# Kernel tuning notes

Measured on AMD Instinct MI355X. Metric: run time of the kernel, lower is better.

The kernel has to match this reference:

```python
import jax, jax.numpy as jnp
import numpy as np
from jax import lax

DN = ('NCHW', 'OIHW', 'NCHW')

def _conv(x, w, b, stride, pad):
    y = lax.conv_general_dilated(x, w, (stride, stride), [(pad, pad), (pad, pad)], dimension_numbers=DN)
    return y + b[None, :, None, None]

def _resblock(x, w1, b1, w2, b2, wd, bd, stride):
    # standard pre-activation-free ResNet block: conv3x3(stride)-ReLU-conv3x3 + 1x1(stride) skip, final ReLU
    identity = _conv(x, wd, bd, stride, 0)
    h = jax.nn.relu(_conv(x, w1, b1, stride, 1))
    h = _conv(h, w2, b2, 1, 1)
    return jax.nn.relu(h + identity)

def _deconv(x, w, b, stride, out_pad):
    # PyTorch ConvTranspose2d(k=3, padding=1, output_padding=out_pad) as dilated conv
    # w has PyTorch layout (in_ch, out_ch, kH, kW) -> flip spatially, swap to OIHW
    wt = jnp.flip(w, (2, 3)).transpose(1, 0, 2, 3)
    y = lax.conv_general_dilated(x, wt, (1, 1), [(1, 1 + out_pad), (1, 1 + out_pad)], lhs_dilation=(stride, stride), dimension_numbers=DN)
    return y + b[None, :, None, None]

def _quantize(enc, codebook):
    # enc: (B, C, H, W); codebook: (N, C). Squared-Euclidean distances, argmin, lookup.
    e = enc.transpose(0, 2, 3, 1)  # (B, H, W, C)
    d = (jnp.sum(e * e, axis=-1, keepdims=True)
         - 2.0 * jnp.einsum('bhwc,nc->bhwn', e, codebook)
         + jnp.sum(codebook * codebook, axis=-1))  # (B, H, W, N)
    idx = jnp.argmin(d, axis=-1)
    q = codebook[idx]  # (B, H, W, C)
    return q.transpose(0, 3, 1, 2)

def setup_inputs() -> dict:
    key = jax.random.key(0)
    ks = jax.random.split(key, 28)
    def W(k, shape):
        return jax.random.normal(k, shape, jnp.float32) * 0.05
    inp = {"x": jax.random.normal(ks[0], (32, 3, 256, 256), jnp.float32)}
    enc_chans = [(3, 64), (64, 128), (128, 64)]
    i = 1
    for l, (cin, cout) in enumerate(enc_chans):
        inp[f"enc{l}_w1"] = W(ks[i], (cout, cin, 3, 3))
        inp[f"enc{l}_b1"] = W(ks[i + 1], (cout,))
        inp[f"enc{l}_w2"] = W(ks[i + 2], (cout, cout, 3, 3))
        inp[f"enc{l}_b2"] = W(ks[i + 3], (cout,))
        inp[f"enc{l}_wd"] = W(ks[i + 4], (cout, cin, 1, 1))
        inp[f"enc{l}_bd"] = W(ks[i + 5], (cout,))
        i += 6
    # decoder ConvTranspose2d weights in PyTorch layout (in_ch, out_ch, 3, 3)
    dec_chans = [(64, 128), (128, 64), (64, 3)]
    for l, (cin, cout) in enumerate(dec_chans):
        inp[f"dec{l}_w"] = W(ks[i], (cin, cout, 3, 3))
        inp[f"dec{l}_b"] = W(ks[i + 1], (cout,))
        i += 2
    inp["codebook"] = W(ks[i], (512, 64))
    return inp

def reference(x, enc0_w1, enc0_b1, enc0_w2, enc0_b2, enc0_wd, enc0_bd,
              enc1_w1, enc1_b1, enc1_w2, enc1_b2, enc1_wd, enc1_bd,
              enc2_w1, enc2_b1, enc2_w2, enc2_b2, enc2_wd, enc2_bd,
              dec0_w, dec0_b, dec1_w, dec1_b, dec2_w, dec2_b, codebook):
    # encode: 256 -> 128 -> 64 -> 64 spatially
    h = _resblock(x, enc0_w1, enc0_b1, enc0_w2, enc0_b2, enc0_wd, enc0_bd, 2)
    h = _resblock(h, enc1_w1, enc1_b1, enc1_w2, enc1_b2, enc1_wd, enc1_bd, 2)
    h = _resblock(h, enc2_w1, enc2_b1, enc2_w2, enc2_b2, enc2_wd, enc2_bd, 1)
    q = _quantize(h, codebook)
    # decode with output_size matching encoder input shapes (output_padding: 0, 1, 1)
    h = jax.nn.relu(_deconv(q, dec0_w, dec0_b, 1, 0))   # 64 -> 64
    h = jax.nn.relu(_deconv(h, dec1_w, dec1_b, 2, 1))   # 64 -> 128
    return _deconv(h, dec2_w, dec2_b, 2, 1)             # 128 -> 256
```

## Files before the change

### kernel.cpp

```cpp
#include <hip/hip_runtime.h>
#include <cstddef>


typedef float v4f __attribute__((ext_vector_type(4)));
typedef _Float16 f16x8 __attribute__((ext_vector_type(8)));
typedef _Float16 f16x4 __attribute__((ext_vector_type(4)));

__device__ __forceinline__ void fma4(v4f& a, float p, const v4f& w) {
    a.x = fmaf(p, w.x, a.x); a.y = fmaf(p, w.y, a.y);
    a.z = fmaf(p, w.z, a.z); a.w = fmaf(p, w.w, a.w);
}

__global__ void repack_k(const float* __restrict__ src, float* __restrict__ dst,
                         int cout, int coutR, int cin, int flip, int deconv)
{
    int t = blockIdx.x * 256 + threadIdx.x;
    int tot = cin * 9 * cout;
    if (t >= tot) return;
    int co = t % cout; int k = (t / cout) % 9; int ci = t / (9 * cout);
    float v = 0.f;
    if (co < coutR) {
        int ks = flip ? 8 - k : k;
        v = deconv ? src[((size_t)ci * coutR + co) * 9 + ks]
                   : src[((size_t)co * cin + ci) * 9 + ks];
    }
    dst[t] = v;
}

__global__ void repackB16_k(const float* __restrict__ src, _Float16* __restrict__ bh,
                            _Float16* __restrict__ bl, int COUT, int CIN, int deconv)
{
    int t = blockIdx.x * 256 + threadIdx.x;
    int tot = 9 * CIN * COUT;
    if (t >= tot) return;
    int NGtot = COUT >> 4, C32 = CIN >> 5;
    int j = t & 7;
    int lane = (t >> 3) & 63;
    int blk = t >> 9;
    int ng = blk % NGtot; blk /= NGtot;
    int c32 = blk % C32;
    int tap = blk / C32;
    int co = ng * 16 + (lane & 15);
    int ci = c32 * 32 + ((lane >> 4) & 3) * 8 + j;
    float v = deconv ? src[((size_t)ci * COUT + co) * 9 + (8 - tap)]
                     : src[((size_t)co * CIN + ci) * 9 + tap];
    _Float16 h = (_Float16)v;
    _Float16 l = (_Float16)(v - (float)h);
    bh[t] = h; bl[t] = l;
}

__global__ void repackW16_k(const float* __restrict__ src, _Float16* __restrict__ wh,
                            _Float16* __restrict__ wl, int COUT, int CIN)
{
    int t = blockIdx.x * 256 + threadIdx.x;
    int tot = CIN * COUT;
    if (t >= tot) return;
    int NGtot = COUT >> 4;
    int j = t & 7;
    int lane = (t >> 3) & 63;
    int blk = t >> 9;
    int ng = blk % NGtot;
    int c32 = blk / NGtot;
    int co = ng * 16 + (lane & 15);
    int ci = c32 * 32 + ((lane >> 4) & 3) * 8 + j;
    float v = src[(size_t)co * CIN + ci];
    _Float16 h = (_Float16)v;
    wh[t] = h; wl[t] = (_Float16)(v - (float)h);
}

__global__ void repackQ_k(const float* __restrict__ cb, _Float16* __restrict__ qb)
{
    int t = blockIdx.x * 256 + threadIdx.x;
    if (t >= 65536) return;
    int j = t & 7;
    int lane = (t >> 3) & 63;
    int hl = (t >> 9) & 1;
    int s = (t >> 10) & 1;
    int nt = t >> 11;
    int code = nt * 16 + (lane & 15);
    int ci = s * 32 + ((lane >> 4) & 3) * 8 + j;
    float v = cb[(size_t)code * 64 + ci];
    _Float16 h = (_Float16)v;
    qb[t] = hl ? (_Float16)(v - (float)h) : h;
}

__global__ void cbnorm_k(const float* __restrict__ cb, float* __restrict__ cn)
{
    int i = blockIdx.x * 256 + threadIdx.x;
    if (i >= 512) return;
    float s = 0.f;
#pragma unroll
    for (int j = 0; j < 64; ++j) { float v = cb[i * 64 + j]; s = fmaf(v, v, s); }
    cn[i] = s;
}

template<int CIN, bool RELU, int ADDMODE, bool CLIN, bool CLOUT>
__launch_bounds__(256, 2)
__global__ void mconv3s1_k(const float* __restrict__ in,
                           const _Float16* __restrict__ Bh, const _Float16* __restrict__ Bl,
                           const float* __restrict__ bias, float* __restrict__ out,
                           const float* __restrict__ addend,
                           int COUT, int H, int W)
{
    constexpr int C32 = CIN / 32;
    __shared__ __align__(16) unsigned char smBuf[76416];
    _Float16* AH = (_Float16*)smBuf;
    _Float16* AL = AH + 12960;
    _Float16* BW = AL + 12960;
    float* smO = (float*)smBuf;

    const int tid = threadIdx.x;
    const int lane = tid & 63, yb = tid >> 6;
    const int n16 = lane & 15, q = lane >> 4;

    int b = blockIdx.x;
    const int chunks = COUT >> 6;
    const int coch = b % chunks; b /= chunks;
    const int tX = W >> 4; const int tx = b % tX; b /= tX;
    const int tY = H >> 4; const int ty = b % tY; const int n = b / tY;
    const int x0 = tx * 16, y0 = ty * 16;
    const int NGtot = COUT >> 4;
    const int ngbase = coch * 4, cobase = coch * 64;

    v4f acc[4][4];
#pragma unroll
    for (int ng = 0; ng < 4; ++ng) {
        float bb = bias[cobase + ng * 16 + n16];
        v4f bv = {bb, bb, bb, bb};
#pragma unroll
        for (int mg = 0; mg < 4; ++mg) acc[mg][ng] = bv;
    }

    for (int c32 = 0; c32 < C32; ++c32) {
        __syncthreads();
        if (CLIN) {
            for (int u = tid; u < 2592; u += 256) {
                int cell = u >> 3, f4 = u & 7;
                int yy = cell / 18, xx = cell - yy * 18;
                int gy = y0 - 1 + yy, gx = x0 - 1 + xx;
                float4 v = make_float4(0.f, 0.f, 0.f, 0.f);
                if (gy >= 0 && gy < H && gx >= 0 && gx < W)
                    v = *(const float4*)&in[(((size_t)n * H + gy) * W + gx) * CIN + c32 * 32 + f4 * 4];
                f16x4 h4, l4;
                h4[0] = (_Float16)v.x; l4[0] = (_Float16)(v.x - (float)h4[0]);
                h4[1] = (_Float16)v.y; l4[1] = (_Float16)(v.y - (float)h4[1]);
                h4[2] = (_Float16)v.z; l4[2] = (_Float16)(v.z - (float)h4[2]);
                h4[3] = (_Float16)v.w; l4[3] = (_Float16)(v.w - (float)h4[3]);
                int a = (yy * 18 + xx) * 40 + f4 * 4;
                *(f16x4*)&AH[a] = h4; *(f16x4*)&AL[a] = l4;
            }
        } else {
            for (int u = tid; u < 10368; u += 256) {
                int ci = u / 324, rem = u - ci * 324;
                int yy = rem / 18, xx = rem - yy * 18;
                int gy = y0 - 1 + yy, gx = x0 - 1 + xx;
                float v = 0.f;
                if (gy >= 0 && gy < H && gx >= 0 && gx < W)
                    v = in[(((size_t)n * CIN + c32 * 32 + ci) * H + gy) * W + gx];
                _Float16 h = (_Float16)v;
                _Float16 l = (_Float16)(v - (float)h);
                int a = (yy * 18 + xx) * 40 + ci;
                AH[a] = h; AL[a] = l;
            }
        }
        for (int ky = 0; ky < 3; ++ky) {
            __syncthreads();
            for (int u = tid; u < 1536; u += 256) {
                int lu = u & 63;
                int rest = u >> 6;
                int hl = rest & 1; rest >>= 1;
                int ng = rest & 3;
                int tapL = rest >> 2;
                const uint4* srcp = (const uint4*)(hl ? Bl : Bh);
                size_t sidx = (((size_t)(ky * 3 + tapL) * C32 + c32) * NGtot + ngbase + ng) * 64 + lu;
                ((uint4*)BW)[u] = srcp[sidx];
            }
            __syncthreads();
#pragma unroll
            for (int kx = 0; kx < 3; ++kx) {
                f16x8 aH[4], aL[4];
#pragma unroll
                for (int mg = 0; mg < 4; ++mg) {
                    int aoff = ((4 * yb + mg + ky) * 18 + n16 + kx) * 40 + q * 8;
                    aH[mg] = *(const f16x8*)&AH[aoff];
                    aL[mg] = *(const f16x8*)&AL[aoff];
                }
                __builtin_amdgcn_s_setprio(1);
#pragma unroll
                for (int ng = 0; ng < 4; ++ng) {
                    int boff = ((kx * 4 + ng) * 2) * 512 + lane * 8;
                    f16x8 bH = *(const f16x8*)&BW[boff];
                    f16x8 bL = *(const f16x8*)&BW[boff + 512];
#pragma unroll
                    for (int mg = 0; mg < 4; ++mg) {
                        acc[mg][ng] = __builtin_amdgcn_mfma_f32_16x16x32_f16(aH[mg], bH, acc[mg][ng], 0, 0, 0);
                        acc[mg][ng] = __builtin_amdgcn_mfma_f32_16x16x32_f16(aL[mg], bH, acc[mg][ng], 0, 0, 0);
                        acc[mg][ng] = __builtin_amdgcn_mfma_f32_16x16x32_f16(aH[mg], bL, acc[mg][ng], 0, 0, 0);
                    }
                }
                __builtin_amdgcn_s_setprio(0);
            }
        }
    }

    __syncthreads();
#pragma unroll
    for (int mg = 0; mg < 4; ++mg)
#pragma unroll
        for (int ng = 0; ng < 4; ++ng) {
            int p = (4 * yb + mg) * 16 + q * 4;
            int co = ng * 16 + n16;
#pragma unroll
            for (int r = 0; r < 4; ++r)
                smO[co * 257 + p + r] = acc[mg][ng][r];
        }
    __syncthreads();
    if (CLOUT) {
        const int p = tid;
        const int py = p >> 4, px = p & 15;
        size_t cellBase = (((size_t)n * H + (y0 + py)) * W + (x0 + px)) * COUT + cobase;
        float* cellp = out + cellBase;
        const float* acell = (ADDMODE == 2) ? addend + cellBase : nullptr;
#pragma unroll
        for (int g = 0; g < 16; ++g) {
            float4 v;
            v.x = smO[(4 * g + 0) * 257 + p];
            v.y = smO[(4 * g + 1) * 257 + p];
            v.z = smO[(4 * g + 2) * 257 + p];
            v.w = smO[(4 * g + 3) * 257 + p];
            if (ADDMODE == 2) {
                float4 a4 = *(const float4*)&acell[4 * g];
                v.x += a4.x; v.y += a4.y; v.z += a4.z; v.w += a4.w;
            }
            if (RELU) {
                v.x = fmaxf(v.x, 0.f); v.y = fmaxf(v.y, 0.f);
                v.z = fmaxf(v.z, 0.f); v.w = fmaxf(v.w, 0.f);
            }
            *(float4*)&cellp[4 * g] = v;
        }
    } else {
        const size_t plane = (size_t)H * W;
        float* ob = out + ((size_t)n * COUT + cobase) * plane;
        const float* ab = (ADDMODE == 1) ? addend + ((size_t)n * COUT + cobase) * plane : nullptr;
#pragma unroll
        for (int k = 0; k < 64; ++k) {
            int e = tid + 256 * k;
            int co = e >> 8, p = e & 255;
            int py = p >> 4, px = p & 15;
            size_t g = (size_t)co * plane + (size_t)(y0 + py) * W + x0 + px;
            float v = smO[co * 257 + p];
            if (ADDMODE == 1) v += ab[g];
            if (RELU) v = fmaxf(v, 0.f);
            ob[g] = v;
        }
    }
}

template<int CIN, int NG, bool RELU>
__launch_bounds__(256, 3)
__global__ void mconv3s2_k(const float* __restrict__ in,
                           const _Float16* __restrict__ Bh, const _Float16* __restrict__ Bl,
                           const float* __restrict__ bias, float* __restrict__ out,
                           const _Float16* __restrict__ Wh, const _Float16* __restrict__ Wl,
                           const float* __restrict__ bias1, float* __restrict__ out1,
                           int COUT, int Hin, int Win)
{
    constexpr int C32 = CIN / 32;
    constexpr int ASZ = 9 * 2 * 17 * 40;
    __shared__ __align__(16) unsigned char smBuf[2 * ASZ * 2];
    _Float16* AH = (_Float16*)smBuf;
    _Float16* AL = AH + ASZ;
    float* smO = (float*)smBuf;

    const int tid = threadIdx.x;
    const int lane = tid & 63, yb = tid >> 6;
    const int n16 = lane & 15, q = lane >> 4;

    const int Hout = Hin >> 1, Wout = Win >> 1;
    int b = blockIdx.x;
    const int chunks = COUT / (NG * 16);
    const int coch = b % chunks; b /= chunks;
    const int tX = Wout >> 4; const int tx = b % tX; b /= tX;
    const int tY = Hout >> 2; const int ty = b % tY; const int n = b / tY;
    const int x0 = tx * 16, y0 = ty * 4;
    const int gx0 = 2 * x0 - 1, gy0 = 2 * y0 - 1;
    const int NGtot = COUT >> 4;
    const int ngbase = coch * NG, cobase = coch * NG * 16;

    v4f acc[NG];
    v4f accW[NG];
#pragma unroll
    for (int ng = 0; ng < NG; ++ng) {
        float bb = bias[cobase + ng * 16 + n16];
        v4f bv = {bb, bb, bb, bb};
        acc[ng] = bv;
        float bw = bias1[cobase + ng * 16 + n16];
        v4f bwv = {bw, bw, bw, bw};
        accW[ng] = bwv;
    }

    const uint4* bhp = (const uint4*)Bh;
    const uint4* blp = (const uint4*)Bl;
    const uint4* whp = (const uint4*)Wh;
    const uint4* wlp = (const uint4*)Wl;

    for (int c32 = 0; c32 < C32; ++c32) {
        __syncthreads();
        for (int u = tid; u < 2376; u += 256) {
            int cell = u >> 3, f4 = u & 7;
            int yy = cell / 33, xx = cell - yy * 33;
            int gy = gy0 + yy, gx = gx0 + xx;
            float4 v = make_float4(0.f, 0.f, 0.f, 0.f);
            if (gy >= 0 && gy < Hin && gx >= 0 && gx < Win)
                v = *(const float4*)&in[(((size_t)n * Hin + gy) * Win + gx) * CIN + c32 * 32 + f4 * 4];
            f16x4 h4, l4;
            h4[0] = (_Float16)v.x; l4[0] = (_Float16)(v.x - (float)h4[0]);
            h4[1] = (_Float16)v.y; l4[1] = (_Float16)(v.y - (float)h4[1]);
            h4[2] = (_Float16)v.z; l4[2] = (_Float16)(v.z - (float)h4[2]);
            h4[3] = (_Float16)v.w; l4[3] = (_Float16)(v.w - (float)h4[3]);
            int a = ((yy * 2 + (xx & 1)) * 17 + (xx >> 1)) * 40 + f4 * 4;
            *(f16x4*)&AH[a] = h4; *(f16x4*)&AL[a] = l4;
        }
        __syncthreads();
#pragma unroll
        for (int ky = 0; ky < 3; ++ky) {
#pragma unroll
            for (int kx = 0; kx < 3; ++kx) {
                const int par = kx & 1, xs = kx >> 1;
                int aoff = (((2 * yb + ky) * 2 + par) * 17 + n16 + xs) * 40 + q * 8;
                f16x8 aH = *(const f16x8*)&AH[aoff];
                f16x8 aL = *(const f16x8*)&AL[aoff];
                size_t sb0 = (((size_t)(ky * 3 + kx) * C32 + c32) * NGtot + ngbase) * 64 + lane;
                __builtin_amdgcn_s_setprio(1);
#pragma unroll
                for (int ng = 0; ng < NG; ++ng) {
                    uint4 rH = bhp[sb0 + (size_t)ng * 64];
                    uint4 rL = blp[sb0 + (size_t)ng * 64];
                    f16x8 bH = *(const f16x8*)&rH;
                    f16x8 bL = *(const f16x8*)&rL;
                    acc[ng] = __builtin_amdgcn_mfma_f32_16x16x32_f16(aH, bH, acc[ng], 0, 0, 0);
                    acc[ng] = __builtin_amdgcn_mfma_f32_16x16x32_f16(aL, bH, acc[ng], 0, 0, 0);
                    acc[ng] = __builtin_amdgcn_mfma_f32_16x16x32_f16(aH, bL, acc[ng], 0, 0, 0);
                }
                __builtin_amdgcn_s_setprio(0);
                if (ky == 1 && kx == 1) {
                    size_t sw0 = ((size_t)c32 * NGtot + ngbase) * 64 + lane;
                    __builtin_amdgcn_s_setprio(1);
#pragma unroll
                    for (int ng = 0; ng < NG; ++ng) {
                        uint4 rH = whp[sw0 + (size_t)ng * 64];
                        uint4 rL = wlp[sw0 + (size_t)ng * 64];
                        f16x8 bH = *(const f16x8*)&rH;
                        f16x8 bL = *(const f16x8*)&rL;
                        accW[ng] = __builtin_amdgcn_mfma_f32_16x16x32_f16(aH, bH, accW[ng], 0, 0, 0);
                        accW[ng] = __builtin_amdgcn_mfma_f32_16x16x32_f16(aL, bH, accW[ng], 0, 0, 0);
                        accW[ng] = __builtin_amdgcn_mfma_f32_16x16x32_f16(aH, bL, accW[ng], 0, 0, 0);
                    }
                    __builtin_amdgcn_s_setprio(0);
                }
            }
        }
    }

    __syncthreads();
#pragma unroll
    for (int ng = 0; ng < NG; ++ng) {
        int co = ng * 16 + n16;
        int p = yb * 16 + q * 4;
#pragma unroll
        for (int r = 0; r < 4; ++r)
            smO[co * 65 + p + r] = acc[ng][r];
    }
    __syncthreads();
    const int p2 = tid >> 2, s2 = tid & 3;
    const int py = p2 >> 4, px = p2 & 15;
    float* cellp = out + ((((size_t)n * Hout + (y0 + py)) * Wout + (x0 + px)) * COUT + s2 * 32);
#pragma unroll
    for (int k = 0; k < 8; ++k) {
        float4 v;
        v.x = smO[(s2 * 32 + 4 * k + 0) * 65 + p2];
        v.y = smO[(s2 * 32 + 4 * k + 1) * 65 + p2];
        v.z = smO[(s2 * 32 + 4 * k + 2) * 65 + p2];
        v.w = smO[(s2 * 32 + 4 * k + 3) * 65 + p2];
        if (RELU) {
            v.x = fmaxf(v.x, 0.f); v.y = fmaxf(v.y, 0.f);
            v.z = fmaxf(v.z, 0.f); v.w = fmaxf(v.w, 0.f);
        }
        *(float4*)&cellp[4 * k] = v;
    }

    __syncthreads();
#pragma unroll
    for (int ng = 0; ng < NG; ++ng) {
        int co = ng * 16 + n16;
        int p = yb * 16 + q * 4;
#pragma unroll
        for (int r = 0; r < 4; ++r)
            smO[co * 65 + p + r] = accW[ng][r];
    }
    __syncthreads();
    float* cellp1 = out1 + ((((size_t)n * Hout + (y0 + py)) * Wout + (x0 + px)) * COUT + s2 * 32);
#pragma unroll
    for (int k = 0; k < 8; ++k) {
        float4 v;
        v.x = smO[(s2 * 32 + 4 * k + 0) * 65 + p2];
        v.y = smO[(s2 * 32 + 4 * k + 1) * 65 + p2];
        v.z = smO[(s2 * 32 + 4 * k + 2) * 65 + p2];
        v.w = smO[(s2 * 32 + 4 * k + 3) * 65 + p2];
        *(float4*)&cellp1[4 * k] = v;
    }
}

template<int CIN, bool RELU>
__launch_bounds__(256, 3)
__global__ void mdeconv2_k(const float* __restrict__ in,
                           const _Float16* __restrict__ Bh, const _Float16* __restrict__ Bl,
                           const float* __restrict__ bias, float* __restrict__ out,
                           int COUT, int Hin, int Win)
{
    constexpr int C32 = CIN / 32;
    __shared__ __align__(16) unsigned char smBuf[38976];
    _Float16* AH = (_Float16*)smBuf;
    _Float16* AL = AH + 3600;
    _Float16* BW = AL + 3600;
    float* smO = (float*)smBuf;

    const int tid = threadIdx.x;
    const int lane = tid & 63, yb = tid >> 6;
    const int n16 = lane & 15, q = lane >> 4;

    int b = blockIdx.x;
    const int chunks = COUT >> 6;
    const int coch = b % chunks; b /= chunks;
    const int tX = Win >> 4; const int tx = b % tX; b /= tX;
    const int tY = Hin >> 2; const int ty = b % tY; const int n = b / tY;
    const int x0 = tx * 16, y0 = ty * 4;
    const int NGtot = COUT >> 4;
    const int ngbase = coch * 4, cobase = coch * 64;

    v4f acc[4][4];
#pragma unroll
    for (int ng = 0; ng < 4; ++ng) {
        float bb = bias[cobase + ng * 16 + n16];
        v4f bv = {bb, bb, bb, bb};
#pragma unroll
        for (int ph = 0; ph < 4; ++ph) acc[ph][ng] = bv;
    }

    for (int c32 = 0; c32 < C32; ++c32) {
        __syncthreads();
        for (int u = tid; u < 680; u += 256) {
            int cell = u >> 3, f4 = u & 7;
            int yy = cell / 17, xx = cell - yy * 17;
            int gy = y0 + yy, gx = x0 + xx;
            float4 v = make_float4(0.f, 0.f, 0.f, 0.f);
            if (gy < Hin && gx < Win)
                v = *(const float4*)&in[(((size_t)n * Hin + gy) * Win + gx) * CIN + c32 * 32 + f4 * 4];
            f16x4 h4, l4;
            h4[0] = (_Float16)v.x; l4[0] = (_Float16)(v.x - (float)h4[0]);
            h4[1] = (_Float16)v.y; l4[1] = (_Float16)(v.y - (float)h4[1]);
            h4[2] = (_Float16)v.z; l4[2] = (_Float16)(v.z - (float)h4[2]);
            h4[3] = (_Float16)v.w; l4[3] = (_Float16)(v.w - (float)h4[3]);
            int a = (yy * 18 + xx) * 40 + f4 * 4;
            *(f16x4*)&AH[a] = h4; *(f16x4*)&AL[a] = l4;
        }
        for (int ky = 0; ky < 3; ++ky) {
            __syncthreads();
            for (int u = tid; u < 1536; u += 256) {
                int lu = u & 63;
                int rest = u >> 6;
                int hl = rest & 1; rest >>= 1;
                int ng = rest & 3;
                int tapL = rest >> 2;
                const uint4* srcp = (const uint4*)(hl ? Bl : Bh);
                size_t sidx = (((size_t)(ky * 3 + tapL) * C32 + c32) * NGtot + ngbase + ng) * 64 + lu;
                ((uint4*)BW)[u] = srcp[sidx];
            }
            __syncthreads();
            const int iy = (ky == 2) ? 1 : 0;
            const int phy = (ky == 1) ? 0 : 2;
#pragma unroll
            for (int kx = 0; kx < 3; ++kx) {
                const int ix = (kx == 2) ? 1 : 0;
                const int ph = phy + ((kx == 1) ? 0 : 1);
                int aoff = ((yb + iy) * 18 + n16 + ix) * 40 + q * 8;
                f16x8 aH = *(const f16x8*)&AH[aoff];
                f16x8 aL = *(const f16x8*)&AL[aoff];
                __builtin_amdgcn_s_setprio(1);
#pragma unroll
                for (int ng = 0; ng < 4; ++ng) {
                    int boff = ((kx * 4 + ng) * 2) * 512 + lane * 8;
                    f16x8 bH = *(const f16x8*)&BW[boff];
                    f16x8 bL = *(const f16x8*)&BW[boff + 512];
                    acc[ph][ng] = __builtin_amdgcn_mfma_f32_16x16x32_f16(aH, bH, acc[ph][ng], 0, 0, 0);
                    acc[ph][ng] = __builtin_amdgcn_mfma_f32_16x16x32_f16(aL, bH, acc[ph][ng], 0, 0, 0);
                    acc[ph][ng] = __builtin_amdgcn_mfma_f32_16x16x32_f16(aH, bL, acc[ph][ng], 0, 0, 0);
                }
                __builtin_amdgcn_s_setprio(0);
            }
        }
    }

    const int Wout = Win * 2;
    const size_t plane = (size_t)(Hin * 2) * (size_t)Wout;
    float* ob = out + ((size_t)n * COUT + cobase) * plane;
    const int oy0 = 2 * y0, ox0 = 2 * x0;
#pragma unroll
    for (int half = 0; half < 2; ++half) {
        __syncthreads();
#pragma unroll
        for (int ph = 0; ph < 4; ++ph) {
            const int dy = ph >> 1, dx = ph & 1;
#pragma unroll
            for (int g = 0; g < 2; ++g) {
                int ng = half * 2 + g;
#pragma unroll
                for (int r = 0; r < 4; ++r)
                    smO[(g * 16 + n16) * 257 + (2 * yb + dy) * 32 + 2 * (q * 4 + r) + dx] = acc[ph][ng][r];
            }
        }
        __syncthreads();
#pragma unroll
        for (int k = 0; k < 32; ++k) {
            int pos = tid;
            int oyl = pos >> 5, oxl = pos & 31;
            float v = smO[k * 257 + pos];
            if (RELU) v = fmaxf(v, 0.f);
            ob[(size_t)(half * 32 + k) * plane + (size_t)(oy0 + oyl) * Wout + ox0 + oxl] = v;
        }
    }
}

template<int CIN, int CB, bool RELU, bool FUSE>
__launch_bounds__(256, 4)
__global__ void conv3s2_k(const float* __restrict__ in, const float* __restrict__ wp,
                          const float* __restrict__ bias, float* __restrict__ out,
                          const float* __restrict__ wd, const float* __restrict__ bd,
                          float* __restrict__ out1,
                          int COUT, int Hin, int Win)
{
    constexpr int COC = 32;
    __shared__ float smIn[CB * 2178];
    __shared__ float smW[CB * 9 * COC];
    __shared__ float smWD[96];
    const int Hout = Hin >> 1, Wout = Win >> 1;
    const int tid = threadIdx.x;
    int b = blockIdx.x;
    const int chunks = COUT / COC;
    const int tX = Wout / 32, tY = Hout / 16;
    const int ch = b % chunks; b /= chunks;
    const int tx = b % tX; b /= tX;
    const int ty = b % tY; const int n = b / tY;
    const int cobase = ch * COC;
    const int r = tid >> 4, c = tid & 15;
    const int gy0 = ty * 32 - 1, gx0 = tx * 64 - 1;

    v4f acc[16];
#pragma unroll
    for (int g = 0; g < 8; ++g) {
        v4f bv = *(const v4f*)&bias[cobase + 4 * g];
        acc[g] = bv; acc[8 + g] = bv;
    }

    const size_t plane = (size_t)Hin * Win;
    const float* ip0 = in + (size_t)n * CIN * plane;
    const float* wp0 = wp + cobase;

    for (int ci0 = 0; ci0 < CIN; ci0 += CB) {
        __syncthreads();
        for (int idx = tid; idx < CB * 2178; idx += 256) {
            int ci = idx / 2178, rem = idx - ci * 2178;
            int rr = rem / 66, cc = rem - rr * 66;
            int gy = gy0 + rr, gx = gx0 + cc;
            float v = 0.f;
            if (gy >= 0 && gy < Hin && gx >= 0 && gx < Win)
                v = ip0[(size_t)(ci0 + ci) * plane + (size_t)gy * Win + gx];
            smIn[idx] = v;
        }
        for (int idx = tid; idx < CB * 9 * COC; idx += 256) {
            int q2 = idx >> 5, co = idx & 31;
            smW[idx] = wp0[((size_t)ci0 * 9 + q2) * COUT + co];
        }
        if (FUSE && tid < 96) {
            int ci = tid >> 5, co = tid & 31;
            smWD[tid] = wd[(size_t)(cobase + co) * 3 + ci];
        }
        __syncthreads();

#pragma unroll 1
        for (int ci = 0; ci < CB; ++ci) {
            float p[15];
            const float* sp = &smIn[ci * 2178 + 2 * r * 66 + 4 * c];
#pragma unroll
            for (int i = 0; i < 3; ++i)
#pragma unroll
                for (int j = 0; j < 5; ++j)
                    p[i * 5 + j] = sp[i * 66 + j];
            const float* wrow = &smW[ci * 288];
#pragma unroll
            for (int k = 0; k < 9; ++k) {
                const int ky = k / 3, kx = k % 3;
#pragma unroll
                for (int g = 0; g < 8; ++g) {
                    v4f wv = *(const v4f*)&wrow[k * 32 + 4 * g];
                    fma4(acc[g],     p[ky * 5 + kx],     wv);
                    fma4(acc[8 + g], p[ky * 5 + kx + 2], wv);
                }
            }
        }
    }

    const int oy = ty * 16 + r, ox = tx * 32 + 2 * c;
    size_t cellBase = (((size_t)n * Hout + oy) * Wout + ox) * COUT + cobase;
#pragma unroll
    for (int g = 0; g < 8; ++g) {
        v4f v0 = acc[g], v1 = acc[8 + g];
        if (RELU) {
#pragma unroll
            for (int e = 0; e < 4; ++e) { v0[e] = fmaxf(v0[e], 0.f); v1[e] = fmaxf(v1[e], 0.f); }
        }
        *(v4f*)&out[cellBase + 4 * g] = v0;
        *(v4f*)&out[cellBase + COUT + 4 * g] = v1;
    }

    if (FUSE) {
        v4f a0[8], a1[8];
#pragma unroll
        for (int g = 0; g < 8; ++g) {
            v4f bv = *(const v4f*)&bd[cobase + 4 * g];
            a0[g] = bv; a1[g] = bv;
        }
#pragma unroll
        for (int ci = 0; ci < CB; ++ci) {
            const float* sp = &smIn[ci * 2178 + 2 * r * 66 + 4 * c];
            float v0 = sp[66 + 1], v1 = sp[66 + 3];
#pragma unroll
            for (int g = 0; g < 8; ++g) {
                v4f wv = *(const v4f*)&smWD[ci * 32 + 4 * g];
                fma4(a0[g], v0, wv);
                fma4(a1[g], v1, wv);
            }
        }
        size_t cb1 = (((size_t)n * Hout + oy) * Wout + ox) * COUT + cobase;
#pragma unroll
        for (int g = 0; g < 8; ++g) {
            *(v4f*)&out1[cb1 + 4 * g] = a0[g];
            *(v4f*)&out1[cb1 + COUT + 4 * g] = a1[g];
        }
    }
}

template<int CIN, int CB, int COC, bool RELU>
__launch_bounds__(256, 3)
__global__ void deconv2_k(const float* __restrict__ in, const float* __restrict__ wp,
                          const float* __restrict__ bias, float* __restrict__ out,
                          int COUTR, int COUTP, int Hin, int Win)
{
    constexpr int RW = 33, RH = 17;
    __shared__ float smIn[CB * RH * RW];
    __shared__ float smW[CB * 9 * COC];
    const int Wout = Win * 2;
    const int tid = threadIdx.x;
    int b = blockIdx.x;
    const int chunks = COUTP / COC;
    const int qTX = Win / 32, qTY = Hin / 16;
    const int ch = b % chunks; b /= chunks;
    const int qtx = b % qTX; b /= qTX;
    const int qty = b % qTY; const int n = b / qTY;
    const int cobase = ch * COC;
    const int tqy = tid >> 4, tqx = tid & 15;
    const int qby = qty * 16, qbx = qtx * 32;

    v4f acc[8 * COC / 4];
#pragma unroll
    for (int g = 0; g < COC / 4; ++g) {
        v4f bv;
#pragma unroll
        for (int e = 0; e < 4; ++e)
            bv[e] = (cobase + 4 * g + e < COUTR) ? bias[cobase + 4 * g + e] : 0.f;
#pragma unroll
        for (int pt = 0; pt < 8; ++pt) acc[pt * (COC / 4) + g] = bv;
    }

    const size_t plane = (size_t)Hin * Win;
    const float* ip0 = in + (size_t)n * CIN * plane;
    const float* wp0 = wp + cobase;

    for (int ci0 = 0; ci0 < CIN; ci0 += CB) {
        __syncthreads();
        for (int idx = tid; idx < CB * RH * RW; idx += 256) {
            int ci = idx / (RH * RW), rem = idx - ci * (RH * RW);
            int rr = rem / RW, cc = rem - rr * RW;
            int gy = qby + rr, gx = qbx + cc;
            float v = 0.f;
            if (gy < Hin && gx < Win)
                v = ip0[(size_t)(ci0 + ci) * plane + (size_t)gy * Win + gx];
            smIn[idx] = v;
        }
        for (int idx = tid; idx < CB * 9 * COC; idx += 256) {
            int q2 = idx / COC, co = idx % COC;
            smW[idx] = wp0[((size_t)ci0 * 9 + q2) * COUTP + co];
        }
        __syncthreads();

#pragma unroll 1
        for (int ci = 0; ci < CB; ++ci) {
            float p[6];
            const float* sp = &smIn[ci * RH * RW + tqy * RW + 2 * tqx];
#pragma unroll
            for (int i = 0; i < 2; ++i)
#pragma unroll
                for (int j = 0; j < 3; ++j)
                    p[i * 3 + j] = sp[i * RW + j];
            const float* wrow = &smW[ci * 9 * COC];
#pragma unroll
            for (int k = 0; k < 9; ++k) {
                const int ky = k / 3, kx = k % 3;
                const int dy = (ky == 1) ? 0 : 1, iy = (ky == 0) ? 1 : 0;
                const int dx = (kx == 1) ? 0 : 1, ix = (kx == 0) ? 1 : 0;
#pragma unroll
                for (int g = 0; g < COC / 4; ++g) {
                    v4f wv = *(const v4f*)&wrow[k * COC + 4 * g];
                    fma4(acc[(0 + dy * 2 + dx) * (COC / 4) + g], p[iy * 3 + ix],     wv);
                    fma4(acc[(4 + dy * 2 + dx) * (COC / 4) + g], p[iy * 3 + ix + 1], wv);
                }
            }
        }
    }

    const size_t oPlane = (size_t)(Hin * 2) * Wout;
    const int oy = 2 * (qby + tqy), ox = 2 * (qbx + 2 * tqx);
#pragma unroll
    for (int g = 0; g < COC / 4; ++g)
#pragma unroll
        for (int e = 0; e < 4; ++e) {
            int cch = cobase + 4 * g + e;
            if (cch >= COUTR) break;
            float* op = out + ((size_t)n * COUTR + cch) * oPlane + (size_t)oy * Wout + ox;
#pragma unroll
            for (int a2 = 0; a2 < 2; ++a2) {
                float u0 = acc[(0 + a2 * 2 + 0) * (COC / 4) + g][e];
                float u1 = acc[(0 + a2 * 2 + 1) * (COC / 4) + g][e];
                float u2 = acc[(4 + a2 * 2 + 0) * (COC / 4) + g][e];
                float u3 = acc[(4 + a2 * 2 + 1) * (COC / 4) + g][e];
                if (RELU) { u0 = fmaxf(u0, 0.f); u1 = fmaxf(u1, 0.f);
                            u2 = fmaxf(u2, 0.f); u3 = fmaxf(u3, 0.f); }
                *(float4*)&op[(size_t)a2 * Wout] = make_float4(u0, u1, u2, u3);
            }
        }
}

template<int CIN, int S, bool RELU, bool CLIN, bool CLOUT>
__launch_bounds__(256, 4)
__global__ void conv1x1_k(const float* __restrict__ in, const float* __restrict__ w,
                          const float* __restrict__ bias, float* __restrict__ out,
                          int COUT, int Hin, int Win, int Hout, int Wout)
{
    constexpr int COC = 32;
    __shared__ float smW[CIN * COC];
    const int tid = threadIdx.x;
    int b = blockIdx.x;
    const int chunks = COUT / COC;
    const int spB = (Hout * Wout) / 256;
    const int ch = b % chunks; b /= chunks;
    const int sb = b % spB; const int n = b / spB;
    const int cobase = ch * COC;

    for (int idx = tid; idx < CIN * COC; idx += 256) {
        int ci = idx / COC, co = idx - ci * COC;
        smW[idx] = w[(size_t)(cobase + co) * CIN + ci];
    }
    __syncthreads();

    const int pos = sb * 256 + tid;
    const int oy = pos / Wout, ox = pos - oy * Wout;

    v4f acc[8];
#pragma unroll
    for (int g = 0; g < 8; ++g) acc[g] = *(const v4f*)&bias[cobase + 4 * g];

    if (CLIN) {
        const float* ip = in + (((size_t)n * Hin + oy * S) * Win + ox * S) * CIN;
#pragma unroll 1
        for (int c4 = 0; c4 < CIN / 4; ++c4) {
            v4f v = *(const v4f*)&ip[c4 * 4];
#pragma unroll
            for (int e = 0; e < 4; ++e)
#pragma unroll
                for (int g = 0; g < 8; ++g)
                    fma4(acc[g], v[e], *(const v4f*)&smW[(c4 * 4 + e) * COC + 4 * g]);
        }
    } else {
        const size_t inPlane = (size_t)Hin * Win;
        const float* ip = in + (size_t)n * CIN * inPlane + (size_t)(oy * S) * Win + (size_t)(ox * S);
#pragma unroll 1
        for (int ci = 0; ci < CIN; ++ci) {
            float v = ip[(size_t)ci * inPlane];
#pragma unroll
            for (int g = 0; g < 8; ++g)
                fma4(acc[g], v, *(const v4f*)&smW[ci * COC + 4 * g]);
        }
    }
    const size_t outPlane = (size_t)Hout * Wout;
    if (CLOUT) {
        size_t cb2 = ((size_t)n * outPlane + pos) * COUT + cobase;
#pragma unroll
        for (int g = 0; g < 8; ++g) {
            v4f v = acc[g];
            if (RELU) {
#pragma unroll
                for (int e = 0; e < 4; ++e) v[e] = fmaxf(v[e], 0.f);
            }
            *(v4f*)&out[cb2 + 4 * g] = v;
        }
    } else {
        float* op = out + ((size_t)n * COUT + cobase) * outPlane + pos;
#pragma unroll
        for (int g = 0; g < 8; ++g)
#pragma unroll
            for (int e = 0; e < 4; ++e) {
                float v = acc[g][e];
                if (RELU) v = fmaxf(v, 0.f);
                op[(size_t)(4 * g + e) * outPlane] = v;
            }
    }
}

__launch_bounds__(256, 4)
__global__ void mquant_k(const float* __restrict__ h, const _Float16* __restrict__ QB,
                         const float* __restrict__ cn, const float* __restrict__ cb,
                         float* __restrict__ q)
{
    __shared__ __align__(16) _Float16 AF[2][8192];
    __shared__ float cns[512];
    __shared__ int bidxs[128];

    const int tid = threadIdx.x;
    const int lane = tid & 63;
    const int wv = tid >> 6;
    const int n16 = lane & 15, qq = lane >> 4;

    const int n = blockIdx.x >> 5;
    const int rem0 = (blockIdx.x & 31) << 7;

    for (int u = tid; u < 1024; u += 256) {
        int posL = u >> 3, grp = u & 7;
        const float* gp = h + ((size_t)n * 4096 + rem0 + posL) * 64 + grp * 8;
        float4 v0 = *(const float4*)gp;
        float4 v1 = *(const float4*)(gp + 4);
        f16x8 hh, ll;
        hh[0] = (_Float16)v0.x; ll[0] = (_Float16)(v0.x - (float)hh[0]);
        hh[1] = (_Float16)v0.y; ll[1] = (_Float16)(v0.y - (float)hh[1]);
        hh[2] = (_Float16)v0.z; ll[2] = (_Float16)(v0.z - (float)hh[2]);
        hh[3] = (_Float16)v0.w; ll[3] = (_Float16)(v0.w - (float)hh[3]);
        hh[4] = (_Float16)v1.x; ll[4] = (_Float16)(v1.x - (float)hh[4]);
        hh[5] = (_Float16)v1.y; ll[5] = (_Float16)(v1.y - (float)hh[5]);
        hh[6] = (_Float16)v1.z; ll[6] = (_Float16)(v1.z - (float)hh[6]);
        hh[7] = (_Float16)v1.w; ll[7] = (_Float16)(v1.w - (float)hh[7]);
        int mt = posL >> 4, s = grp >> 2, qv = grp & 3;
        int a = ((mt * 2 + s) * 64 + (posL & 15) + qv * 16) * 8;
        *(f16x8*)&AF[0][a] = hh;
        *(f16x8*)&AF[1][a] = ll;
    }
    for (int u = tid; u < 512; u += 256) cns[u] = cn[u];
    __syncthreads();

    f16x8 aH[2][2], aL[2][2];
#pragma unroll
    for (int m = 0; m < 2; ++m)
#pragma unroll
        for (int s = 0; s < 2; ++s) {
            int a = (((wv * 2 + m) * 2 + s) * 64 + lane) * 8;
            aH[m][s] = *(const f16x8*)&AF[0][a];
            aL[m][s] = *(const f16x8*)&AF[1][a];
        }

    float best[2][4]; int bi[2][4];
#pragma unroll
    for (int m = 0; m < 2; ++m)
#pragma unroll
        for (int r = 0; r < 4; ++r) { best[m][r] = 3.4e38f; bi[m][r] = 0; }

    const uint4* qbp = (const uint4*)QB;
#pragma unroll 1
    for (int nt = 0; nt < 32; ++nt) {
        uint4 rH0 = qbp[((nt * 2 + 0) * 2 + 0) * 64 + lane];
        uint4 rL0 = qbp[((nt * 2 + 0) * 2 + 1) * 64 + lane];
        uint4 rH1 = qbp[((nt * 2 + 1) * 2 + 0) * 64 + lane];
        uint4 rL1 = qbp[((nt * 2 + 1) * 2 + 1) * 64 + lane];
        f16x8 bH0 = *(const f16x8*)&rH0;
        f16x8 bL0 = *(const f16x8*)&rL0;
        f16x8 bH1 = *(const f16x8*)&rH1;
        f16x8 bL1 = *(const f16x8*)&rL1;
        float cnv = cns[nt * 16 + n16];
        const int code = nt * 16 + n16;
        __builtin_amdgcn_s_setprio(1);
#pragma unroll
        for (int m = 0; m < 2; ++m) {
            v4f acc = {0.f, 0.f, 0.f, 0.f};
            acc = __builtin_amdgcn_mfma_f32_16x16x32_f16(aH[m][0], bH0, acc, 0, 0, 0);
            acc = __builtin_amdgcn_mfma_f32_16x16x32_f16(aL[m][0], bH0, acc, 0, 0, 0);
            acc = __builtin_amdgcn_mfma_f32_16x16x32_f16(aH[m][0], bL0, acc, 0, 0, 0);
            acc = __builtin_amdgcn_mfma_f32_16x16x32_f16(aH[m][1], bH1, acc, 0, 0, 0);
            acc = __builtin_amdgcn_mfma_f32_16x16x32_f16(aL[m][1], bH1, acc, 0, 0, 0);
            acc = __builtin_amdgcn_mfma_f32_16x16x32_f16(aH[m][1], bL1, acc, 0, 0, 0);
#pragma unroll
            for (int r = 0; r < 4; ++r) {
                float d = fmaf(-2.f, acc[r], cnv);
                if (d < best[m][r]) { best[m][r] = d; bi[m][r] = code; }
            }
        }
        __builtin_amdgcn_s_setprio(0);
    }

#pragma unroll
    for (int m = 0; m < 2; ++m)
#pragma unroll
        for (int r = 0; r < 4; ++r) {
#pragma unroll
            for (int msk = 1; msk < 16; msk <<= 1) {
                float ob = __shfl_xor(best[m][r], msk);
                int oi = __shfl_xor(bi[m][r], msk);
                if (ob < best[m][r] || (ob == best[m][r] && oi < bi[m][r])) {
                    best[m][r] = ob; bi[m][r] = oi;
                }
            }
            if (n16 == 0) bidxs[wv * 32 + m * 16 + qq * 4 + r] = bi[m][r];
        }
    __syncthreads();

    const int p = tid & 127, jh = tid >> 7;
    const int code = bidxs[p];
    const float4* crow4 = (const float4*)(cb + (size_t)code * 64);
    float4* qp4 = (float4*)(q + ((size_t)n * 4096 + rem0 + p) * 64);
#pragma unroll
    for (int k = 0; k < 8; ++k)
        qp4[jh * 8 + k] = crow4[jh * 8 + k];
}

extern "C" void kernel_launch(void* const* d_in, const int* in_sizes, int n_in,
                              void* d_out, int out_size, void* d_ws, size_t ws_size,
                              hipStream_t stream)
{
    const float* x    = (const float*)d_in[0];
    const float* e0w1 = (const float*)d_in[1];  const float* e0b1 = (const float*)d_in[2];
    const float* e0w2 = (const float*)d_in[3];  const float* e0b2 = (const float*)d_in[4];
    const float* e0wd = (const float*)d_in[5];  const float* e0bd = (const float*)d_in[6];
    const float* e1w1 = (const float*)d_in[7];  const float* e1b1 = (const float*)d_in[8];
    const float* e1w2 = (const float*)d_in[9];  const float* e1b2 = (const float*)d_in[10];
    const float* e1wd = (const float*)d_in[11]; const float* e1bd = (const float*)d_in[12];
    const float* e2w1 = (const float*)d_in[13]; const float* e2b1 = (const float*)d_in[14];
    const float* e2w2 = (const float*)d_in[15]; const float* e2b2 = (const float*)d_in[16];
    const float* e2wd = (const float*)d_in[17]; const float* e2bd = (const float*)d_in[18];
    const float* d0w  = (const float*)d_in[19]; const float* d0b  = (const float*)d_in[20];
    const float* d1w  = (const float*)d_in[21]; const float* d1b  = (const float*)d_in[22];
    const float* d2w  = (const float*)d_in[23]; const float* d2b  = (const float*)d_in[24];
    const float* cb   = (const float*)d_in[25];
    float* out = (float*)d_out;
    float* ws  = (float*)d_ws;

    float* P_e0w1 = out + 0;
    _Float16* Bh_d1   = (_Float16*)(out + 1728);
    _Float16* Bl_d1   = (_Float16*)(out + 38592);
    _Float16* Bh_e0c2 = (_Float16*)(out + 77760);
    _Float16* Bl_e0c2 = (_Float16*)(out + 96192);
    _Float16* Bh_e1c2 = (_Float16*)(out + 114624);
    _Float16* Bl_e1c2 = (_Float16*)(out + 188352);
    _Float16* Bh_e2c1 = (_Float16*)(out + 262080);
    _Float16* Bl_e2c1 = (_Float16*)(out + 298944);
    _Float16* Bh_e2c2 = (_Float16*)(out + 335808);
    _Float16* Bl_e2c2 = (_Float16*)(out + 354240);
    _Float16* Bh_d0   = (_Float16*)(out + 372672);
    _Float16* Bl_d0   = (_Float16*)(out + 409536);
    _Float16* Bh_e1c1 = (_Float16*)(out + 446400);
    _Float16* Bl_e1c1 = (_Float16*)(out + 483264);
    _Float16* QB = (_Float16*)(out + 520128);
    float* CN = out + 552896;
    _Float16* Wh_e1d = (_Float16*)(out + 553408);
    _Float16* Wl_e1d = (_Float16*)(out + 557504);
    float* P_d2w  = ws + 50405376;

    float* S0 = ws;
    float* T1 = ws + 33554432;
    float* T3 = ws + 33554432;
    float* S1 = ws + 50331648;
    float* S2 = ws;
    float* T5 = ws + 8388608;
    float* Q  = ws + 16777216;
    float* D0 = ws + 33554432;
    float* D1 = ws;

    dim3 blk(256);
    auto rp = [&](const float* src, float* dst, int cout, int coutR, int cin, int flip, int dec) {
        int tot = cin * 9 * cout;
        repack_k<<<dim3((tot + 255) / 256), blk, 0, stream>>>(src, dst, cout, coutR, cin, flip, dec);
    };
    auto rpB = [&](const float* src, _Float16* bh, _Float16* bl, int cout, int cin, int dec) {
        int tot = 9 * cin * cout;
        repackB16_k<<<dim3((tot + 255) / 256), blk, 0, stream>>>(src, bh, bl, cout, cin, dec);
    };

    rp(e0w1, P_e0w1, 64, 64, 3, 0, 0);
    rpB(e0w2, Bh_e0c2, Bl_e0c2, 64, 64, 0);
    rpB(e1w1, Bh_e1c1, Bl_e1c1, 128, 64, 0);
    rpB(e1w2, Bh_e1c2, Bl_e1c2, 128, 128, 0);
    rpB(e2w1, Bh_e2c1, Bl_e2c1, 64, 128, 0);
    rpB(e2w2, Bh_e2c2, Bl_e2c2, 64, 64, 0);
    rpB(d0w,  Bh_d0,   Bl_d0,   128, 64, 1);
    rpB(d1w,  Bh_d1,   Bl_d1,   64, 128, 1);
    repackW16_k<<<dim3(32), blk, 0, stream>>>(e1wd, Wh_e1d, Wl_e1d, 128, 64);
    repackQ_k<<<dim3(256), blk, 0, stream>>>(cb, QB);
    cbnorm_k<<<dim3(2), blk, 0, stream>>>(cb, CN);

    conv3s2_k<3, 3, true, true><<<dim3(32 * 8 * 4 * 2), blk, 0, stream>>>(
        x, P_e0w1, e0b1, T1, e0wd, e0bd, S0, 64, 256, 256);
    mconv3s1_k<64, true, 2, true, true><<<dim3(32 * 8 * 8 * 1), blk, 0, stream>>>(
        T1, Bh_e0c2, Bl_e0c2, e0b2, S0, S0, 64, 128, 128);

    mconv3s2_k<64, 8, true><<<dim3(32 * 16 * 4), blk, 0, stream>>>(
        S0, Bh_e1c1, Bl_e1c1, e1b1, T3, Wh_e1d, Wl_e1d, e1bd, S1, 128, 128, 128);
    mconv3s1_k<128, true, 2, true, true><<<dim3(32 * 4 * 4 * 2), blk, 0, stream>>>(
        T3, Bh_e1c2, Bl_e1c2, e1b2, S1, S1, 128, 64, 64);

    conv1x1_k<128, 1, false, true, true><<<dim3(32 * 16 * 2), blk, 0, stream>>>(
        S1, e2wd, e2bd, S2, 64, 64, 64, 64, 64);
    mconv3s1_k<128, true, 0, true, true><<<dim3(32 * 4 * 4 * 1), blk, 0, stream>>>(
        S1, Bh_e2c1, Bl_e2c1, e2b1, T5, nullptr, 64, 64, 64);
    rp(d2w, P_d2w, 4, 3, 64, 0, 1);
    mconv3s1_k<64, true, 2, true, true><<<dim3(32 * 4 * 4 * 1), blk, 0, stream>>>(
        T5, Bh_e2c2, Bl_e2c2, e2b2, S2, S2, 64, 64, 64);

    mquant_k<<<dim3(1024), blk, 0, stream>>>(S2, QB, CN, cb, Q);

    mconv3s1_k<64, true, 0, true, true><<<dim3(32 * 4 * 4 * 2), blk, 0, stream>>>(
        Q, Bh_d0, Bl_d0, d0b, D0, nullptr, 128, 64, 64);

    mdeconv2_k<128, true><<<dim3(32 * 16 * 4), blk, 0, stream>>>(
        D0, Bh_d1, Bl_d1, d1b, D1, 64, 64, 64);

    deconv2_k<64, 8, 4, false><<<dim3(32 * 4 * 8), blk, 0, stream>>>(
        D1, P_d2w, d2b, out, 3, 4, 128, 128);
}
```

Baseline: 1.309 ms.

## Move first strided 3x3 conv onto MFMA with im2col and split-fp16 precision

Replaces the scalar FMA first-layer stride-2 conv (3 input channels) with an MFMA kernel. It builds an im2col tile in shared memory with K=27 padded to 32 and uses hi/lo fp16 splitting to keep near-fp32 accuracy. The fused 1x1 stride-2 skip conv is still computed with scalar FMAs from cached center pixels. A new repack kernel lays out the weights in MFMA fragment order. The cost is three MFMAs per product, wasted padding lanes, and an irregular scatter when filling the im2col tile.

```diff
diff --git a/kernel.cpp b/kernel.cpp
--- a/kernel.cpp
+++ b/kernel.cpp
@@ -68,6 +68,23 @@
     wh[t] = h; wl[t] = (_Float16)(v - (float)h);
 }
 
+__global__ void repackB0_k(const float* __restrict__ src, _Float16* __restrict__ bh,
+                           _Float16* __restrict__ bl)
+{
+    int t = blockIdx.x * 256 + threadIdx.x;
+    if (t >= 4096) return;
+    int j = t & 7, lane = (t >> 3) & 63, ng = t >> 9;
+    int co = ng * 16 + (lane & 15);
+    int k = ((lane >> 4) & 3) * 8 + j;
+    float v = 0.f;
+    if (k < 27) {
+        int tap = k / 3, ci = k - 3 * tap;
+        v = src[(size_t)(co * 3 + ci) * 9 + tap];
+    }
+    _Float16 h = (_Float16)v;
+    bh[t] = h; bl[t] = (_Float16)(v - (float)h);
+}
+
 __global__ void repackQ_k(const float* __restrict__ cb, _Float16* __restrict__ qb)
 {
     int t = blockIdx.x * 256 + threadIdx.x;
@@ -92,6 +109,143 @@
 #pragma unroll
     for (int j = 0; j < 64; ++j) { float v = cb[i * 64 + j]; s = fmaf(v, v, s); }
     cn[i] = s;
+}
+
+__launch_bounds__(256, 3)
+__global__ void mconv0_k(const float* __restrict__ x,
+                         const _Float16* __restrict__ Bh, const _Float16* __restrict__ Bl,
+                         const float* __restrict__ bias, float* __restrict__ out,
+                         const float* __restrict__ wd, const float* __restrict__ bd,
+                         float* __restrict__ out1)
+{
+    __shared__ __align__(16) unsigned char smBuf[44800];
+    _Float16* AH = (_Float16*)smBuf;
+    _Float16* AL = AH + 10240;
+    float* smWD = (float*)(smBuf + 40960);
+    float* smC  = (float*)(smBuf + 41728);
+    float* smO  = (float*)smBuf;
+
+    const int tid = threadIdx.x;
+    const int lane = tid & 63, yb = tid >> 6;
+    const int n16 = lane & 15, q = lane >> 4;
+
+    int b = blockIdx.x;
+    const int tx = b & 7; b >>= 3;
+    const int ty = b & 7; const int n = b >> 3;
+    const int x0 = tx * 16, y0 = ty * 16;
+    const int wy0 = 2 * y0 - 1, wx0 = 2 * x0 - 1;
+
+    v4f acc[4][4];
+#pragma unroll
+    for (int ng = 0; ng < 4; ++ng) {
+        float bb = bias[ng * 16 + n16];
+        v4f bv = {bb, bb, bb, bb};
+#pragma unroll
+        for (int mg = 0; mg < 4; ++mg) acc[mg][ng] = bv;
+    }
+
+    if (tid < 192) smWD[tid] = wd[(size_t)(tid & 63) * 3 + (tid >> 6)];
+    for (int u = tid; u < 1280; u += 256) {
+        int pos = u / 5, k = 27 + (u - (u / 5) * 5);
+        AH[pos * 40 + k] = (_Float16)0.f;
+        AL[pos * 40 + k] = (_Float16)0.f;
+    }
+    for (int u = tid; u < 3267; u += 256) {
+        int ci = u / 1089, rem = u - ci * 1089;
+        int ly = rem / 33, lx = rem - ly * 33;
+        int gy = wy0 + ly, gx = wx0 + lx;
+        float v = 0.f;
+        if (gy >= 0 && gy < 256 && gx >= 0 && gx < 256)
+            v = x[((size_t)(n * 3 + ci) * 256 + gy) * 256 + gx];
+        _Float16 h = (_Float16)v;
+        _Float16 l = (_Float16)(v - (float)h);
+#pragma unroll
+        for (int tyk = 0; tyk < 3; ++tyk) {
+            int dy = ly - tyk;
+            if (dy < 0 || (dy & 1)) continue;
+            int py = dy >> 1; if (py > 15) continue;
+#pragma unroll
+            for (int txk = 0; txk < 3; ++txk) {
+                int dx = lx - txk;
+                if (dx < 0 || (dx & 1)) continue;
+                int px = dx >> 1; if (px > 15) continue;
+                int a = (py * 16 + px) * 40 + (tyk * 3 + txk) * 3 + ci;
+                AH[a] = h; AL[a] = l;
+            }
+        }
+        if ((ly & 1) && (lx & 1))
+            smC[((ly >> 1) * 16 + (lx >> 1)) * 3 + ci] = v;
+    }
+    __syncthreads();
+
+    f16x8 aH[4], aL[4];
+#pragma unroll
+    for (int mg = 0; mg < 4; ++mg) {
+        int pos = (4 * yb + mg) * 16 + n16;
+        aH[mg] = *(const f16x8*)&AH[pos * 40 + q * 8];
+        aL[mg] = *(const f16x8*)&AL[pos * 40 + q * 8];
+    }
+    const uint4* bhp = (const uint4*)Bh;
+    const uint4* blp = (const uint4*)Bl;
+    __builtin_amdgcn_s_setprio(1);
+#pragma unroll
+    for (int ng = 0; ng < 4; ++ng) {
+        uint4 rH = bhp[ng * 64 + lane];
+        uint4 rL = blp[ng * 64 + lane];
+        f16x8 bH = *(const f16x8*)&rH;
+        f16x8 bL = *(const f16x8*)&rL;
+#pragma unroll
+        for (int mg = 0; mg < 4; ++mg) {
+            acc[mg][ng] = __builtin_amdgcn_mfma_f32_16x16x32_f16(aH[mg], bH, acc[mg][ng], 0, 0, 0);
+            acc[mg][ng] = __builtin_amdgcn_mfma_f32_16x16x32_f16(aL[mg], bH, acc[mg][ng], 0, 0, 0);
+            acc[mg][ng] = __builtin_amdgcn_mfma_f32_16x16x32_f16(aH[mg], bL, acc[mg][ng], 0, 0, 0);
+        }
+    }
+    __builtin_amdgcn_s_setprio(0);
+
+    const int p = tid, py = p >> 4, px = p & 15;
+#pragma unroll
+    for (int half = 0; half < 2; ++half) {
+        __syncthreads();
+#pragma unroll
+        for (int g2 = 0; g2 < 2; ++g2) {
+            int ng = half * 2 + g2;
+            int row = g2 * 16 + n16;
+#pragma unroll
+            for (int mg = 0; mg < 4; ++mg) {
+                int pp = (4 * yb + mg) * 16 + q * 4;
+#pragma unroll
+                for (int r = 0; r < 4; ++r)
+                    smO[row * 257 + pp + r] = acc[mg][ng][r];
+            }
+        }
+        __syncthreads();
+        size_t cellBase = (((size_t)n * 128 + (y0 + py)) * 128 + (x0 + px)) * 64 + half * 32;
+#pragma unroll
+        for (int g = 0; g < 8; ++g) {
+            float4 v;
+            v.x = fmaxf(smO[(4 * g + 0) * 257 + p], 0.f);
+            v.y = fmaxf(smO[(4 * g + 1) * 257 + p], 0.f);
+            v.z = fmaxf(smO[(4 * g + 2) * 257 + p], 0.f);
+            v.w = fmaxf(smO[(4 * g + 3) * 257 + p], 0.f);
+            *(float4*)&out[cellBase + 4 * g] = v;
+        }
+    }
+
+    v4f a8[16];
+#pragma unroll
+    for (int g = 0; g < 16; ++g) a8[g] = *(const v4f*)&bd[4 * g];
+    float c0 = smC[p * 3 + 0], c1 = smC[p * 3 + 1], c2 = smC[p * 3 + 2];
+#pragma unroll
+    for (int g = 0; g < 16; ++g) {
+        fma4(a8[g], c0, *(const v4f*)&smWD[0 * 64 + 4 * g]);
+        fma4(a8[g], c1, *(const v4f*)&smWD[1 * 64 + 4 * g]);
+        fma4(a8[g], c2, *(const v4f*)&smWD[2 * 64 + 4 * g]);
+    }
+    size_t cb1 = (((size_t)n * 128 + (y0 + py)) * 128 + (x0 + px)) * 64;
+#pragma unroll
+    for (int g = 0; g < 16; ++g)
+        *(v4f*)&out1[cb1 + 4 * g] = a8[g];
 }
 
 template<int CIN, bool RELU, int ADDMODE, bool CLIN, bool CLOUT>
@@ -241,7 +395,7 @@
     } else {
         const size_t plane = (size_t)H * W;
         float* ob = out + ((size_t)n * COUT + cobase) * plane;
-        const float* ab = (ADDMODE == 1) ? addend + ((size_t)n * COUT + cobase) * plane : nullptr;
+        const float* ab = nullptr;
 #pragma unroll
         for (int k = 0; k < 64; ++k) {
             int e = tid + 256 * k;
@@ -249,7 +403,6 @@
             int py = p >> 4, px = p & 15;
             size_t g = (size_t)co * plane + (size_t)(y0 + py) * W + x0 + px;
             float v = smO[co * 257 + p];
-            if (ADDMODE == 1) v += ab[g];
             if (RELU) v = fmaxf(v, 0.f);
             ob[g] = v;
         }
@@ -527,125 +680,6 @@
             float v = smO[k * 257 + pos];
             if (RELU) v = fmaxf(v, 0.f);
             ob[(size_t)(half * 32 + k) * plane + (size_t)(oy0 + oyl) * Wout + ox0 + oxl] = v;
-        }
-    }
-}
-
-template<int CIN, int CB, bool RELU, bool FUSE>
-__launch_bounds__(256, 4)
-__global__ void conv3s2_k(const float* __restrict__ in, const float* __restrict__ wp,
-                          const float* __restrict__ bias, float* __restrict__ out,
-                          const float* __restrict__ wd, const float* __restrict__ bd,
-                          float* __restrict__ out1,
-                          int COUT, int Hin, int Win)
-{
-    constexpr int COC = 32;
-    __shared__ float smIn[CB * 2178];
-    __shared__ float smW[CB * 9 * COC];
-    __shared__ float smWD[96];
-    const int Hout = Hin >> 1, Wout = Win >> 1;
-    const int tid = threadIdx.x;
-    int b = blockIdx.x;
-    const int chunks = COUT / COC;
-    const int tX = Wout / 32, tY = Hout / 16;
-    const int ch = b % chunks; b /= chunks;
-    const int tx = b % tX; b /= tX;
-    const int ty = b % tY; const int n = b / tY;
-    const int cobase = ch * COC;
-    const int r = tid >> 4, c = tid & 15;
-    const int gy0 = ty * 32 - 1, gx0 = tx * 64 - 1;
-
-    v4f acc[16];
-#pragma unroll
-    for (int g = 0; g < 8; ++g) {
-        v4f bv = *(const v4f*)&bias[cobase + 4 * g];
-        acc[g] = bv; acc[8 + g] = bv;
-    }
-
-    const size_t plane = (size_t)Hin * Win;
-    const float* ip0 = in + (size_t)n * CIN * plane;
-    const float* wp0 = wp + cobase;
-
-    for (int ci0 = 0; ci0 < CIN; ci0 += CB) {
-        __syncthreads();
-        for (int idx = tid; idx < CB * 2178; idx += 256) {
-            int ci = idx / 2178, rem = idx - ci * 2178;
-            int rr = rem / 66, cc = rem - rr * 66;
-            int gy = gy0 + rr, gx = gx0 + cc;
-            float v = 0.f;
-            if (gy >= 0 && gy < Hin && gx >= 0 && gx < Win)
-                v = ip0[(size_t)(ci0 + ci) * plane + (size_t)gy * Win + gx];
-            smIn[idx] = v;
-        }
-        for (int idx = tid; idx < CB * 9 * COC; idx += 256) {
-            int q2 = idx >> 5, co = idx & 31;
-            smW[idx] = wp0[((size_t)ci0 * 9 + q2) * COUT + co];
-        }
-        if (FUSE && tid < 96) {
-            int ci = tid >> 5, co = tid & 31;
-            smWD[tid] = wd[(size_t)(cobase + co) * 3 + ci];
-        }
-        __syncthreads();
-
-#pragma unroll 1
-        for (int ci = 0; ci < CB; ++ci) {
-            float p[15];
-            const float* sp = &smIn[ci * 2178 + 2 * r * 66 + 4 * c];
-#pragma unroll
-            for (int i = 0; i < 3; ++i)
-#pragma unroll
-                for (int j = 0; j < 5; ++j)
-                    p[i * 5 + j] = sp[i * 66 + j];
-            const float* wrow = &smW[ci * 288];
-#pragma unroll
-            for (int k = 0; k < 9; ++k) {
-                const int ky = k / 3, kx = k % 3;
-#pragma unroll
-                for (int g = 0; g < 8; ++g) {
-                    v4f wv = *(const v4f*)&wrow[k * 32 + 4 * g];
-                    fma4(acc[g],     p[ky * 5 + kx],     wv);
-                    fma4(acc[8 + g], p[ky * 5 + kx + 2], wv);
-                }
-            }
-        }
-    }
-
-    const int oy = ty * 16 + r, ox = tx * 32 + 2 * c;
-    size_t cellBase = (((size_t)n * Hout + oy) * Wout + ox) * COUT + cobase;
-#pragma unroll
-    for (int g = 0; g < 8; ++g) {
-        v4f v0 = acc[g], v1 = acc[8 + g];
-        if (RELU) {
-#pragma unroll
-            for (int e = 0; e < 4; ++e) { v0[e] = fmaxf(v0[e], 0.f); v1[e] = fmaxf(v1[e], 0.f); }
-        }
-        *(v4f*)&out[cellBase + 4 * g] = v0;
-        *(v4f*)&out[cellBase + COUT + 4 * g] = v1;
-    }
-
-    if (FUSE) {
-        v4f a0[8], a1[8];
-#pragma unroll
-        for (int g = 0; g < 8; ++g) {
-            v4f bv = *(const v4f*)&bd[cobase + 4 * g];
-            a0[g] = bv; a1[g] = bv;
-        }
-#pragma unroll
-        for (int ci = 0; ci < CB; ++ci) {
-            const float* sp = &smIn[ci * 2178 + 2 * r * 66 + 4 * c];
-            float v0 = sp[66 + 1], v1 = sp[66 + 3];
-#pragma unroll
-            for (int g = 0; g < 8; ++g) {
-                v4f wv = *(const v4f*)&smWD[ci * 32 + 4 * g];
-                fma4(a0[g], v0, wv);
-                fma4(a1[g], v1, wv);
-            }
-        }
-        size_t cb1 = (((size_t)n * Hout + oy) * Wout + ox) * COUT + cobase;
-#pragma unroll
-        for (int g = 0; g < 8; ++g) {
-            *(v4f*)&out1[cb1 + 4 * g] = a0[g];
-            *(v4f*)&out1[cb1 + COUT + 4 * g] = a1[g];
         }
     }
 }
@@ -959,7 +993,6 @@
     float* out = (float*)d_out;
     float* ws  = (float*)d_ws;
 
-    float* P_e0w1 = out + 0;
     _Float16* Bh_d1   = (_Float16*)(out + 1728);
     _Float16* Bl_d1   = (_Float16*)(out + 38592);
     _Float16* Bh_e0c2 = (_Float16*)(out + 77760);
@@ -978,6 +1011,8 @@
     float* CN = out + 552896;
     _Float16* Wh_e1d = (_Float16*)(out + 553408);
     _Float16* Wl_e1d = (_Float16*)(out + 557504);
+    _Float16* Bh0 = (_Float16*)(out + 561600);
+    _Float16* Bl0 = (_Float16*)(out + 563648);
     float* P_d2w  = ws + 50405376;
 
     float* S0 = ws;
@@ -1000,7 +1035,7 @@
         repackB16_k<<<dim3((tot + 255) / 256), blk, 0, stream>>>(src, bh, bl, cout, cin, dec);
     };
 
-    rp(e0w1, P_e0w1, 64, 64, 3, 0, 0);
+    repackB0_k<<<dim3(16), blk, 0, stream>>>(e0w1, Bh0, Bl0);
     rpB(e0w2, Bh_e0c2, Bl_e0c2, 64, 64, 0);
     rpB(e1w1, Bh_e1c1, Bl_e1c1, 128, 64, 0);
     rpB(e1w2, Bh_e1c2, Bl_e1c2, 128, 128, 0);
@@ -1012,8 +1047,8 @@
     repackQ_k<<<dim3(256), blk, 0, stream>>>(cb, QB);
     cbnorm_k<<<dim3(2), blk, 0, stream>>>(cb, CN);
 
-    conv3s2_k<3, 3, true, true><<<dim3(32 * 8 * 4 * 2), blk, 0, stream>>>(
-        x, P_e0w1, e0b1, T1, e0wd, e0bd, S0, 64, 256, 256);
+    mconv0_k<<<dim3(32 * 8 * 8), blk, 0, stream>>>(
+        x, Bh0, Bl0, e0b1, T1, e0wd, e0bd, S0);
     mconv3s1_k<64, true, 2, true, true><<<dim3(32 * 8 * 8 * 1), blk, 0, stream>>>(
         T1, Bh_e0c2, Bl_e0c2, e0b2, S0, S0, 64, 128, 128);
 
```

Measured after the change: 1.314 ms. No clear change (+0.4%).
